# Kernel tuning notes

Hardware: AMD Instinct MI355X
Metric: run time of the kernel (lower is better)

Reference implementation:

```python
import jax, jax.numpy as jnp
import numpy as np

NEG_SLOPE = 0.2
NUM_GRAPHS = 64


def _gatv2_layer(x, src, dst, Wl, bl, Wr, br, att, bias, n_nodes, heads, ch):
    # lin_l (source) and lin_r (target) transforms -> [N, H, C]
    xs = (x @ Wl + bl).reshape(n_nodes, heads, ch)
    xd = (x @ Wr + br).reshape(n_nodes, heads, ch)
    s = xs[src]                                   # [E, H, C] gathered source feats
    e = jax.nn.leaky_relu(s + xd[dst], NEG_SLOPE)  # GATv2: leaky_relu BEFORE att dot
    score = jnp.einsum('ehc,hc->eh', e, att)       # [E, H]
    # segment softmax over edges sharing the same target node
    smax = jax.ops.segment_max(score, dst, num_segments=n_nodes)
    ex = jnp.exp(score - smax[dst])
    denom = jax.ops.segment_sum(ex, dst, num_segments=n_nodes)
    alpha = ex / denom[dst]                        # [E, H]
    out = jax.ops.segment_sum(alpha[:, :, None] * s, dst, num_segments=n_nodes)
    return out.reshape(n_nodes, heads * ch) + bias


def setup_inputs() -> dict:
    key = jax.random.key(0)
    ks = jax.random.split(key, 20)
    N, E, F = 50000, 800000, 128
    H, C = 4, 64
    G = NUM_GRAPHS
    sc = 0.05
    inp = {
        'x': jax.random.normal(ks[0], (N, F), jnp.float32),
        'edge_index': jax.random.randint(ks[1], (2, E), 0, N, jnp.int64 if jax.config.read('jax_enable_x64') else jnp.int32).astype(jnp.int32),
        'batch': jnp.sort(jax.random.randint(ks[2], (N,), 0, G)).astype(jnp.int32),
        'W_l1': jax.random.normal(ks[3], (F, H * C)) * sc,
        'b_l1': jax.random.normal(ks[4], (H * C,)) * sc,
        'W_r1': jax.random.normal(ks[5], (F, H * C)) * sc,
        'b_r1': jax.random.normal(ks[6], (H * C,)) * sc,
        'att1': jax.random.normal(ks[7], (H, C)) * sc,
        'bias1': jax.random.normal(ks[8], (H * C,)) * sc,
        'W_l2': jax.random.normal(ks[9], (H * C, C)) * sc,
        'b_l2': jax.random.normal(ks[10], (C,)) * sc,
        'W_r2': jax.random.normal(ks[11], (H * C, C)) * sc,
        'b_r2': jax.random.normal(ks[12], (C,)) * sc,
        'att2': jax.random.normal(ks[13], (1, C)) * sc,
        'bias2': jax.random.normal(ks[14], (C,)) * sc,
        'W_lin': jax.random.normal(ks[15], (C, 1)) * sc,
        'b_lin': jax.random.normal(ks[16], (1,)) * sc,
    }
    return inp


def reference(x, edge_index, batch, W_l1, b_l1, W_r1, b_r1, att1, bias1,
              W_l2, b_l2, W_r2, b_r2, att2, bias2, W_lin, b_lin):
    N = x.shape[0]
    # PyG GATv2Conv adds self-loops by default
    loops = jnp.arange(N, dtype=edge_index.dtype)
    src = jnp.concatenate([edge_index[0], loops])
    dst = jnp.concatenate([edge_index[1], loops])

    h = _gatv2_layer(x, src, dst, W_l1, b_l1, W_r1, b_r1, att1, bias1, N, 4, 64)
    h = jax.nn.relu(h)  # dropout=identity (eval), norm=Identity
    h = _gatv2_layer(h, src, dst, W_l2, b_l2, W_r2, b_r2, att2, bias2, N, 1, 64)

    # global mean pool over graphs
    sums = jax.ops.segment_sum(h, batch, num_segments=NUM_GRAPHS)
    counts = jax.ops.segment_sum(jnp.ones((N,), h.dtype), batch, num_segments=NUM_GRAPHS)
    pooled = sums / jnp.maximum(counts, 1.0)[:, None]  # [G, 64]
    return pooled @ W_lin + b_lin                      # [G, 1]
```

## Files before the change

kernel.cpp:

```cpp
#include <hip/hip_runtime.h>
#include <hip/hip_bf16.h>
#include <math.h>

typedef __attribute__((ext_vector_type(8))) short short8;
typedef __attribute__((ext_vector_type(4))) float floatx4;

__device__ __forceinline__ float bf2f(unsigned short u) {
  union { unsigned int i; float f; } v; v.i = ((unsigned int)u) << 16; return v.f;
}
__device__ __forceinline__ unsigned short f2bf(float f) {
  union { float f; unsigned int u; } v; v.f = f;
  unsigned int r = (v.u + 0x7fffu + ((v.u >> 16) & 1u)) >> 16;
  return (unsigned short)r;
}
__device__ __forceinline__ int imin(int a, int b) { return a < b ? a : b; }
__device__ __forceinline__ int iclamp(int v, int lo, int hi) {
  return v < lo ? lo : (v > hi ? hi : v);
}
__device__ __forceinline__ float uasf(unsigned int u) {
  union { unsigned int i; float f; } v; v.i = u; return v.f;
}
__device__ __forceinline__ float sum16(float x) {
  union { float f; int i; } a, t;
  a.f = x;
  t.i = __builtin_amdgcn_update_dpp(0, a.i, 0x121, 0xF, 0xF, true); a.f += t.f;
  t.i = __builtin_amdgcn_update_dpp(0, a.i, 0x122, 0xF, 0xF, true); a.f += t.f;
  t.i = __builtin_amdgcn_update_dpp(0, a.i, 0x124, 0xF, 0xF, true); a.f += t.f;
  t.i = __builtin_amdgcn_update_dpp(0, a.i, 0x128, 0xF, 0xF, true); a.f += t.f;
  return a.f;
}

__global__ void k_sentinel(float* out, float val) {
  if (threadIdx.x < 64) out[threadIdx.x] = val;
}

struct CvtSegs {
  const void* src[10];
  unsigned short* dst[10];
  int len[10];
};

__global__ void k_prep(const void* __restrict__ x, unsigned short* __restrict__ x_c,
                       int n8, CvtSegs segs,
                       const void* __restrict__ s0, const void* __restrict__ s1,
                       const void* __restrict__ s2, const void* __restrict__ s3,
                       unsigned short* __restrict__ d0, unsigned short* __restrict__ d1,
                       unsigned short* __restrict__ d2, unsigned short* __restrict__ d3,
                       const int* __restrict__ edst, int* deg, int E, int N,
                       int* dflag, int* colx, int ET, int nCvt8, int nTransB) {
  __shared__ int csh;
  if (threadIdx.x == 0) csh = 0;
  __syncthreads();
  {
    unsigned short u = ((const unsigned short*)x)[threadIdx.x];
    int e = (u >> 7) & 0xFF;
    atomicAdd(&csh, (u == 0) || (e >= 100 && e <= 145));
  }
  __syncthreads();
  int isf = (csh < 240);

  int b = blockIdx.x;
  if (b < nCvt8) {
    if (!isf) return;
    int i = b * 256 + threadIdx.x;
    if (i >= n8) return;
    const float* s = (const float*)x + (size_t)i * 8;
    ushort4 a, c;
    a.x = f2bf(s[0]); a.y = f2bf(s[1]); a.z = f2bf(s[2]); a.w = f2bf(s[3]);
    c.x = f2bf(s[4]); c.y = f2bf(s[5]); c.z = f2bf(s[6]); c.w = f2bf(s[7]);
    ((ushort4*)x_c)[i * 2] = a;
    ((ushort4*)x_c)[i * 2 + 1] = c;
    return;
  }
  b -= nCvt8;
  if (b < 10) {
    if (b == 0) {
      if (threadIdx.x == 0) dflag[0] = isf;
      if (threadIdx.x >= 240) colx[ET + (threadIdx.x - 240)] = 0;
    }
    int i = threadIdx.x;
    if (i < segs.len[b])
      segs.dst[b][i] = isf ? f2bf(((const float*)segs.src[b])[i])
                           : ((const unsigned short*)segs.src[b])[i];
    return;
  }
  b -= 10;
  if (b < nTransB) {
    int idx = b * 256 + threadIdx.x;
    const void* src; unsigned short* dst; int R, C, loc;
    if (idx < 32768)      { src = s0; dst = d0; R = 128; C = 256; loc = idx; }
    else if (idx < 65536) { src = s1; dst = d1; R = 128; C = 256; loc = idx - 32768; }
    else if (idx < 81920) { src = s2; dst = d2; R = 256; C = 64;  loc = idx - 65536; }
    else                  { src = s3; dst = d3; R = 256; C = 64;  loc = idx - 81920; }
    unsigned short u = isf ? f2bf(((const float*)src)[loc])
                           : ((const unsigned short*)src)[loc];
    int r = loc / C, cc = loc - r * C;
    dst[cc * R + r] = u;
    return;
  }
  b -= nTransB;
  int base = b * 1024 + threadIdx.x;
#pragma unroll
  for (int k = 0; k < 4; ++k) {
    int e = base + k * 256;
    if (e < E) atomicAdd(&deg[iclamp(edst[e], 0, N - 1)], 1);
  }
}

__global__ __launch_bounds__(1024) void k_scan1(const int* __restrict__ deg, int* bsum, int N) {
  __shared__ int sm[1024];
  int tid = threadIdx.x;
  int i = blockIdx.x * 1024 + tid;
  sm[tid] = (i < N) ? deg[i] + 1 : 0;
  __syncthreads();
  for (int off = 512; off > 0; off >>= 1) {
    if (tid < off) sm[tid] += sm[tid + off];
    __syncthreads();
  }
  if (tid == 0) bsum[blockIdx.x] = sm[0];
}

__global__ __launch_bounds__(1024) void k_scan3(const int* __restrict__ deg,
                                                const int* __restrict__ bsum,
                                                int* rowptr, int* cursor, int N) {
  __shared__ int sm[1024];
  __shared__ int boff;
  int tid = threadIdx.x;
  if (tid == 0) {
    int r = 0;
    for (int b = 0; b < blockIdx.x; ++b) r += bsum[b];
    boff = r;
  }
  int i = blockIdx.x * 1024 + tid;
  int v = (i < N) ? deg[i] + 1 : 0;
  sm[tid] = v;
  __syncthreads();
  for (int off = 1; off < 1024; off <<= 1) {
    int t = (tid >= off) ? sm[tid - off] : 0;
    __syncthreads();
    sm[tid] += t;
    __syncthreads();
  }
  if (i < N) {
    int ex = sm[tid] - v + boff;
    rowptr[i] = ex;
    cursor[i] = ex;
    if (i == N - 1) rowptr[N] = ex + v;
  }
}

template <int K, int CT, int RT>
__device__ __forceinline__ void gemm2r_body(
    int bx, int by, int tid,
    const unsigned short* __restrict__ A,
    const unsigned short* __restrict__ BTl, const unsigned short* __restrict__ BTr,
    const unsigned short* __restrict__ bl, const unsigned short* __restrict__ br,
    unsigned short* __restrict__ outl, unsigned short* __restrict__ outr,
    int Nrows, int M) {
  constexpr int KI = K / 32;
  int lane = tid & 63;
  int wave = tid >> 6;
  int r = lane & 15, q = lane >> 4;
  int col0 = by * (4 * CT * 16) + wave * (CT * 16);
  int row0 = bx * (16 * RT);
  short8 Bl[KI][CT], Br[KI][CT];
#pragma unroll
  for (int t = 0; t < CT; ++t) {
    const unsigned short* bpl = BTl + (size_t)(col0 + t * 16 + r) * K + q * 8;
    const unsigned short* bpr = BTr + (size_t)(col0 + t * 16 + r) * K + q * 8;
#pragma unroll
    for (int k = 0; k < KI; ++k) {
      Bl[k][t] = *reinterpret_cast<const short8*>(bpl + k * 32);
      Br[k][t] = *reinterpret_cast<const short8*>(bpr + k * 32);
    }
  }
  float bvl[CT], bvr[CT];
#pragma unroll
  for (int t = 0; t < CT; ++t) {
    bvl[t] = bf2f(bl[col0 + t * 16 + r]);
    bvr[t] = bf2f(br[col0 + t * 16 + r]);
  }
  short8 a[KI], an[KI];
  {
    int ar0 = imin(row0 + r, Nrows - 1);
    const unsigned short* Ap = A + (size_t)ar0 * K + q * 8;
#pragma unroll
    for (int k = 0; k < KI; ++k) a[k] = *reinterpret_cast<const short8*>(Ap + k * 32);
  }
  for (int rt = 0; rt < RT; ++rt) {
    if (rt + 1 < RT) {
      int arn = imin(row0 + (rt + 1) * 16 + r, Nrows - 1);
      const unsigned short* Apn = A + (size_t)arn * K + q * 8;
#pragma unroll
      for (int k = 0; k < KI; ++k) an[k] = *reinterpret_cast<const short8*>(Apn + k * 32);
    }
    floatx4 accl[CT], accr[CT];
#pragma unroll
    for (int t = 0; t < CT; ++t) {
      accl[t] = (floatx4){0.f, 0.f, 0.f, 0.f};
      accr[t] = (floatx4){0.f, 0.f, 0.f, 0.f};
    }
#pragma unroll
    for (int k = 0; k < KI; ++k) {
#pragma unroll
      for (int t = 0; t < CT; ++t) {
        accl[t] = __builtin_amdgcn_mfma_f32_16x16x32_bf16(a[k], Bl[k][t], accl[t], 0, 0, 0);
        accr[t] = __builtin_amdgcn_mfma_f32_16x16x32_bf16(a[k], Br[k][t], accr[t], 0, 0, 0);
      }
    }
#pragma unroll
    for (int t = 0; t < CT; ++t) {
      int col = col0 + t * 16 + r;
#pragma unroll
      for (int rr = 0; rr < 4; ++rr) {
        int row = row0 + rt * 16 + q * 4 + rr;
        if (row < Nrows) {
          outl[(size_t)row * M + col] = f2bf(accl[t][rr] + bvl[t]);
          outr[(size_t)row * M + col] = f2bf(accr[t][rr] + bvr[t]);
        }
      }
    }
#pragma unroll
    for (int k = 0; k < KI; ++k) a[k] = an[k];
  }
}

__global__ __launch_bounds__(256) void k_phase1(
    const unsigned short* __restrict__ A0, const unsigned short* __restrict__ A1,
    const int* __restrict__ dflag,
    const unsigned short* __restrict__ BTl, const unsigned short* __restrict__ BTr,
    const unsigned short* __restrict__ bl, const unsigned short* __restrict__ br,
    unsigned short* __restrict__ outl, unsigned short* __restrict__ outr,
    int Nrows, int M, int nG, int nS,
    const int* __restrict__ esrc, const int* __restrict__ edst,
    const int* __restrict__ rowptr, int* cursor, int* colx, int E, int N) {
  int b = blockIdx.x;
  int m2 = 2 * imin(nG, nS);
  bool isG;
  int idx;
  if (b < m2) { isG = (b & 1) == 0; idx = b >> 1; }
  else        { isG = nG > nS;      idx = imin(nG, nS) + (b - m2); }
  if (isG) {
    const unsigned short* A = dflag[0] ? A1 : A0;
    gemm2r_body<128, 2, 8>(idx >> 1, idx & 1, threadIdx.x, A, BTl, BTr, bl, br,
                           outl, outr, Nrows, M);
    return;
  }
  int ET = E + N;
  int base = idx * 1024 + threadIdx.x;
#pragma unroll
  for (int k = 0; k < 4; ++k) {
    int e = base + k * 256;
    if (e < ET) {
      if (e < E) {
        int s = iclamp(esrc[e], 0, N - 1), d = iclamp(edst[e], 0, N - 1);
        int pos = atomicAdd(&cursor[d], 1);
        colx[iclamp(pos, 0, ET - 1)] = s;
      } else {
        int i = e - E;
        colx[rowptr[i + 1] - 1] = i;
      }
    }
  }
}

__global__ __launch_bounds__(256) void k_gemm2r_l2(
    const unsigned short* __restrict__ A,
    const unsigned short* __restrict__ BTl, const unsigned short* __restrict__ BTr,
    const unsigned short* __restrict__ bl, const unsigned short* __restrict__ br,
    unsigned short* __restrict__ outl, unsigned short* __restrict__ outr,
    int Nrows, int M) {
  gemm2r_body<256, 1, 4>(blockIdx.x, 0, threadIdx.x, A, BTl, BTr, bl, br,
                         outl, outr, Nrows, M);
}

#define UNPACK2(u, v0, v1, v2, v3)          \
  v0 = uasf(u.x << 16); v1 = uasf(u.x & 0xffff0000u); \
  v2 = uasf(u.y << 16); v3 = uasf(u.y & 0xffff0000u);

#define SCORE(q0, q1, q2, q3, p)                             \
  p = q0 * 0.6f;                                             \
  p = fmaf(q1, 0.6f, p); p = fmaf(q2, 0.6f, p); p = fmaf(q3, 0.6f, p); \
  p = fmaf(c0, fabsf(q0), p); p = fmaf(c1, fabsf(q1), p);    \
  p = fmaf(c2, fabsf(q2), p); p = fmaf(c3, fabsf(q3), p);

__global__ __launch_bounds__(256) void k_agg_h4(
    const int* __restrict__ rowptr, const int* __restrict__ colx,
    const unsigned short* __restrict__ xs, const unsigned short* __restrict__ xd,
    const unsigned short* __restrict__ att, const unsigned short* __restrict__ bias,
    unsigned short* __restrict__ hout, int N) {
  int lane = threadIdx.x & 63;
  int dst = (blockIdx.x * 256 + threadIdx.x) >> 6;
  if (dst >= N) return;
  int off = lane << 2;
  unsigned int off2 = (unsigned int)off * 2;
  const char* xsb = (const char*)xs;
  ushort4 au = *reinterpret_cast<const ushort4*>(att + off);
  ushort4 du = *reinterpret_cast<const ushort4*>(xd + (size_t)dst * 256 + off);
  float a0 = bf2f(au.x), a1 = bf2f(au.y), a2 = bf2f(au.z), a3 = bf2f(au.w);
  float d0 = bf2f(du.x), d1 = bf2f(du.y), d2 = bf2f(du.z), d3 = bf2f(du.w);
  float ad0 = a0 * d0, ad1 = a1 * d1, ad2 = a2 * d2, ad3 = a3 * d3;
  float c0 = copysignf(0.4f, a0), c1 = copysignf(0.4f, a1);
  float c2 = copysignf(0.4f, a2), c3 = copysignf(0.4f, a3);
  float l = 0.f, o0 = 0.f, o1 = 0.f, o2 = 0.f, o3 = 0.f;
  int beg = __builtin_amdgcn_readfirstlane(rowptr[dst]);
  int end = __builtin_amdgcn_readfirstlane(rowptr[dst + 1]);
  int p0 = colx[beg], p1 = colx[beg + 1], p2 = colx[beg + 2], p3 = colx[beg + 3];
  uint2 ua = *(const uint2*)(xsb + (((unsigned)p0 << 9) + off2));
  uint2 ub = *(const uint2*)(xsb + (((unsigned)p1 << 9) + off2));
  uint2 uc = *(const uint2*)(xsb + (((unsigned)p2 << 9) + off2));
  uint2 ud = *(const uint2*)(xsb + (((unsigned)p3 << 9) + off2));
  int q0 = 0, q1 = 0, q2 = 0, q3 = 0;
  if (beg + 4 < end) {
    q0 = colx[beg + 4]; q1 = colx[beg + 5]; q2 = colx[beg + 6]; q3 = colx[beg + 7];
  }
  for (int e = beg; e < end; e += 4) {
    uint2 na = ua, nb = ub, nc = uc, nd = ud;
    if (e + 4 < end) {
      na = *(const uint2*)(xsb + (((unsigned)q0 << 9) + off2));
      nb = *(const uint2*)(xsb + (((unsigned)q1 << 9) + off2));
      nc = *(const uint2*)(xsb + (((unsigned)q2 << 9) + off2));
      nd = *(const uint2*)(xsb + (((unsigned)q3 << 9) + off2));
    }
    if (e + 8 < end) {
      q0 = colx[e + 8]; q1 = colx[e + 9]; q2 = colx[e + 10]; q3 = colx[e + 11];
    }
    float va0, va1, va2, va3, vb0, vb1, vb2, vb3;
    float vc0, vc1, vc2, vc3, vd0, vd1, vd2, vd3;
    UNPACK2(ua, va0, va1, va2, va3)
    UNPACK2(ub, vb0, vb1, vb2, vb3)
    UNPACK2(uc, vc0, vc1, vc2, vc3)
    UNPACK2(ud, vd0, vd1, vd2, vd3)
    float qa0 = fmaf(a0, va0, ad0), qa1 = fmaf(a1, va1, ad1);
    float qa2 = fmaf(a2, va2, ad2), qa3 = fmaf(a3, va3, ad3);
    float qb0 = fmaf(a0, vb0, ad0), qb1 = fmaf(a1, vb1, ad1);
    float qb2 = fmaf(a2, vb2, ad2), qb3 = fmaf(a3, vb3, ad3);
    float qc0 = fmaf(a0, vc0, ad0), qc1 = fmaf(a1, vc1, ad1);
    float qc2 = fmaf(a2, vc2, ad2), qc3 = fmaf(a3, vc3, ad3);
    float qd0 = fmaf(a0, vd0, ad0), qd1 = fmaf(a1, vd1, ad1);
    float qd2 = fmaf(a2, vd2, ad2), qd3 = fmaf(a3, vd3, ad3);
    float pa, pb, pc, pd;
    SCORE(qa0, qa1, qa2, qa3, pa)
    SCORE(qb0, qb1, qb2, qb3, pb)
    SCORE(qc0, qc1, qc2, qc3, pc)
    SCORE(qd0, qd1, qd2, qd3, pd)
    pa = sum16(pa); pb = sum16(pb); pc = sum16(pc); pd = sum16(pd);
    pa = fminf(pa, 60.f);
    pb = (e + 1 < end) ? fminf(pb, 60.f) : -INFINITY;
    pc = (e + 2 < end) ? fminf(pc, 60.f) : -INFINITY;
    pd = (e + 3 < end) ? fminf(pd, 60.f) : -INFINITY;
    float wa = __expf(pa), wb = __expf(pb), wc = __expf(pc), wd = __expf(pd);
    l += (wa + wb) + (wc + wd);
    o0 = fmaf(wa, va0, o0); o0 = fmaf(wb, vb0, o0);
    o0 = fmaf(wc, vc0, o0); o0 = fmaf(wd, vd0, o0);
    o1 = fmaf(wa, va1, o1); o1 = fmaf(wb, vb1, o1);
    o1 = fmaf(wc, vc1, o1); o1 = fmaf(wd, vd1, o1);
    o2 = fmaf(wa, va2, o2); o2 = fmaf(wb, vb2, o2);
    o2 = fmaf(wc, vc2, o2); o2 = fmaf(wd, vd2, o2);
    o3 = fmaf(wa, va3, o3); o3 = fmaf(wb, vb3, o3);
    o3 = fmaf(wc, vc3, o3); o3 = fmaf(wd, vd3, o3);
    ua = na; ub = nb; uc = nc; ud = nd;
  }
  float rl = 1.0f / l;
  ushort4 bu = *reinterpret_cast<const ushort4*>(bias + off);
  ushort4 res;
  res.x = f2bf(fmaxf(fmaf(o0, rl, bf2f(bu.x)), 0.f));
  res.y = f2bf(fmaxf(fmaf(o1, rl, bf2f(bu.y)), 0.f));
  res.z = f2bf(fmaxf(fmaf(o2, rl, bf2f(bu.z)), 0.f));
  res.w = f2bf(fmaxf(fmaf(o3, rl, bf2f(bu.w)), 0.f));
  *reinterpret_cast<ushort4*>(hout + (size_t)dst * 256 + off) = res;
}

__global__ __launch_bounds__(256) void k_agg_h1(
    const int* __restrict__ rowptr, const int* __restrict__ colx,
    const unsigned short* __restrict__ xs, const unsigned short* __restrict__ xd,
    const unsigned short* __restrict__ att, const unsigned short* __restrict__ bias,
    float* __restrict__ hout, int N) {
  int lane = threadIdx.x & 63;
  int wid = (blockIdx.x * 256 + threadIdx.x) >> 6;
  int g = lane >> 4, sl = lane & 15;
  int dst = wid * 4 + g;
  bool valid = dst < N;
  int dsafe = valid ? dst : 0;
  int cb = sl << 2;
  unsigned int cb2 = (unsigned int)cb * 2;
  const char* xsb = (const char*)xs;
  ushort4 au = *reinterpret_cast<const ushort4*>(att + cb);
  ushort4 du = *reinterpret_cast<const ushort4*>(xd + (size_t)dsafe * 64 + cb);
  float a0 = bf2f(au.x), a1 = bf2f(au.y), a2 = bf2f(au.z), a3 = bf2f(au.w);
  float d0 = bf2f(du.x), d1 = bf2f(du.y), d2 = bf2f(du.z), d3 = bf2f(du.w);
  float ad0 = a0 * d0, ad1 = a1 * d1, ad2 = a2 * d2, ad3 = a3 * d3;
  float c0 = copysignf(0.4f, a0), c1 = copysignf(0.4f, a1);
  float c2 = copysignf(0.4f, a2), c3 = copysignf(0.4f, a3);
  float l = 0.f, o0 = 0.f, o1 = 0.f, o2 = 0.f, o3 = 0.f;
  int beg = valid ? rowptr[dst] : 0;
  int end = valid ? rowptr[dst + 1] : 0;
  if (end > beg) {
    int p0 = colx[beg], p1 = colx[beg + 1], p2 = colx[beg + 2], p3 = colx[beg + 3];
    uint2 ua = *(const uint2*)(xsb + (((unsigned)p0 << 7) + cb2));
    uint2 ub = *(const uint2*)(xsb + (((unsigned)p1 << 7) + cb2));
    uint2 uc = *(const uint2*)(xsb + (((unsigned)p2 << 7) + cb2));
    uint2 ud = *(const uint2*)(xsb + (((unsigned)p3 << 7) + cb2));
    int q0 = 0, q1 = 0, q2 = 0, q3 = 0;
    if (beg + 4 < end) {
      q0 = colx[beg + 4]; q1 = colx[beg + 5]; q2 = colx[beg + 6]; q3 = colx[beg + 7];
    }
    for (int e = beg; e < end; e += 4) {
      uint2 na = ua, nb = ub, nc = uc, nd = ud;
      if (e + 4 < end) {
        na = *(const uint2*)(xsb + (((unsigned)q0 << 7) + cb2));
        nb = *(const uint2*)(xsb + (((unsigned)q1 << 7) + cb2));
        nc = *(const uint2*)(xsb + (((unsigned)q2 << 7) + cb2));
        nd = *(const uint2*)(xsb + (((unsigned)q3 << 7) + cb2));
      }
      if (e + 8 < end) {
        q0 = colx[e + 8]; q1 = colx[e + 9]; q2 = colx[e + 10]; q3 = colx[e + 11];
      }
      float va0, va1, va2, va3, vb0, vb1, vb2, vb3;
      float vc0, vc1, vc2, vc3, vd0, vd1, vd2, vd3;
      UNPACK2(ua, va0, va1, va2, va3)
      UNPACK2(ub, vb0, vb1, vb2, vb3)
      UNPACK2(uc, vc0, vc1, vc2, vc3)
      UNPACK2(ud, vd0, vd1, vd2, vd3)
      float qa0 = fmaf(a0, va0, ad0), qa1 = fmaf(a1, va1, ad1);
      float qa2 = fmaf(a2, va2, ad2), qa3 = fmaf(a3, va3, ad3);
      float qb0 = fmaf(a0, vb0, ad0), qb1 = fmaf(a1, vb1, ad1);
      float qb2 = fmaf(a2, vb2, ad2), qb3 = fmaf(a3, vb3, ad3);
      float qc0 = fmaf(a0, vc0, ad0), qc1 = fmaf(a1, vc1, ad1);
      float qc2 = fmaf(a2, vc2, ad2), qc3 = fmaf(a3, vc3, ad3);
      float qd0 = fmaf(a0, vd0, ad0), qd1 = fmaf(a1, vd1, ad1);
      float qd2 = fmaf(a2, vd2, ad2), qd3 = fmaf(a3, vd3, ad3);
      float pa, pb, pc, pd;
      SCORE(qa0, qa1, qa2, qa3, pa)
      SCORE(qb0, qb1, qb2, qb3, pb)
      SCORE(qc0, qc1, qc2, qc3, pc)
      SCORE(qd0, qd1, qd2, qd3, pd)
      pa = sum16(pa); pb = sum16(pb); pc = sum16(pc); pd = sum16(pd);
      pa = fminf(pa, 60.f);
      pb = (e + 1 < end) ? fminf(pb, 60.f) : -INFINITY;
      pc = (e + 2 < end) ? fminf(pc, 60.f) : -INFINITY;
      pd = (e + 3 < end) ? fminf(pd, 60.f) : -INFINITY;
      float wa = __expf(pa), wb = __expf(pb), wc = __expf(pc), wd = __expf(pd);
      l += (wa + wb) + (wc + wd);
      o0 = fmaf(wa, va0, o0); o0 = fmaf(wb, vb0, o0);
      o0 = fmaf(wc, vc0, o0); o0 = fmaf(wd, vd0, o0);
      o1 = fmaf(wa, va1, o1); o1 = fmaf(wb, vb1, o1);
      o1 = fmaf(wc, vc1, o1); o1 = fmaf(wd, vd1, o1);
      o2 = fmaf(wa, va2, o2); o2 = fmaf(wb, vb2, o2);
      o2 = fmaf(wc, vc2, o2); o2 = fmaf(wd, vd2, o2);
      o3 = fmaf(wa, va3, o3); o3 = fmaf(wb, vb3, o3);
      o3 = fmaf(wc, vc3, o3); o3 = fmaf(wd, vd3, o3);
      ua = na; ub = nb; uc = nc; ud = nd;
    }
  }
  if (valid) {
    float rl = 1.0f / l;
    ushort4 bu = *reinterpret_cast<const ushort4*>(bias + cb);
    floatx4 res;
    res[0] = fmaf(o0, rl, bf2f(bu.x));
    res[1] = fmaf(o1, rl, bf2f(bu.y));
    res[2] = fmaf(o2, rl, bf2f(bu.z));
    res[3] = fmaf(o3, rl, bf2f(bu.w));
    *reinterpret_cast<floatx4*>(hout + (size_t)dst * 64 + cb) = res;
  }
}

__global__ __launch_bounds__(256) void k_pool(const float* __restrict__ h2,
                                              const int* __restrict__ batch,
                                              float* pool, int* cnt, int N) {
  int lane = threadIdx.x & 63;
  int wid = (blockIdx.x * 256 + threadIdx.x) >> 6;
  int n0 = wid * 32;
  if (n0 >= N) return;
  int nend = imin(n0 + 32, N);
  float acc = 0.f;
  int c = 0;
  int gcur = iclamp(batch[n0], 0, 63);
  for (int n = n0; n < nend; ++n) {
    int gg = iclamp(batch[n], 0, 63);
    if (gg != gcur) {
      atomicAdd(&pool[gcur * 64 + lane], acc);
      if (lane == 0) atomicAdd(&cnt[gcur], c);
      acc = 0.f; c = 0; gcur = gg;
    }
    acc += h2[(size_t)n * 64 + lane];
    c++;
  }
  atomicAdd(&pool[gcur * 64 + lane], acc);
  if (lane == 0) atomicAdd(&cnt[gcur], c);
}

__global__ void k_final(const float* __restrict__ pool, const int* __restrict__ cnt,
                        const unsigned short* __restrict__ Wlinc,
                        const unsigned short* __restrict__ blinc,
                        float* __restrict__ out) {
  int g = threadIdx.x;
  if (g >= 64) return;
  float inv = 1.f / fmaxf((float)cnt[g], 1.f);
  float s = 0.f;
  for (int c = 0; c < 64; ++c) s += pool[g * 64 + c] * bf2f(Wlinc[c]);
  out[g] = fmaf(s, inv, bf2f(blinc[0]));
}

extern "C" void kernel_launch(void* const* d_in, const int* in_sizes, int n_in,
                              void* d_out, int out_size, void* d_ws, size_t ws_size,
                              hipStream_t stream) {
  const void* x     = d_in[0];
  const int*  ei    = (const int*)d_in[1];
  const int*  batch = (const int*)d_in[2];
  const void* Wl1 = d_in[3];  const void* bl1 = d_in[4];
  const void* Wr1 = d_in[5];  const void* br1 = d_in[6];
  const void* att1 = d_in[7]; const void* bias1 = d_in[8];
  const void* Wl2 = d_in[9];  const void* bl2 = d_in[10];
  const void* Wr2 = d_in[11]; const void* br2 = d_in[12];
  const void* att2 = d_in[13]; const void* bias2 = d_in[14];
  const void* Wlin = d_in[15]; const void* blin = d_in[16];
  float* out = (float*)d_out;

  const int F = 128, HC = 256, C2 = 64;
  int N = in_sizes[0] / F;
  int E = in_sizes[1] / 2;
  int ET = E + N;
  const int* esrc = ei;
  const int* edst = ei + E;

  char* w = (char*)d_ws;
  auto alloc = [&](size_t bytes) {
    char* p = w;
    w += (bytes + 255) & ~(size_t)255;
    return p;
  };
  int* dflag  = (int*)alloc(4);
  int* rowptr = (int*)alloc((size_t)(N + 1) * 4);
  int* cursor = (int*)alloc((size_t)N * 4);
  int* bsum   = (int*)alloc(1024 * 4);
  int* colx   = (int*)alloc((size_t)(ET + 16) * 4);
  unsigned short* smallc = (unsigned short*)alloc(4096);
  unsigned short* Wl1T = (unsigned short*)alloc((size_t)F * HC * 2);
  unsigned short* Wr1T = (unsigned short*)alloc((size_t)F * HC * 2);
  unsigned short* Wl2T = (unsigned short*)alloc((size_t)HC * C2 * 2);
  unsigned short* Wr2T = (unsigned short*)alloc((size_t)HC * C2 * 2);
  int* deg    = (int*)alloc((size_t)N * 4);
  float* pool = (float*)alloc(64 * 64 * 4);
  int* cnt    = (int*)alloc(64 * 4);
  unsigned short* xs1  = (unsigned short*)alloc((size_t)N * HC * 2);
  unsigned short* xd1  = (unsigned short*)alloc((size_t)N * HC * 2);
  unsigned short* h1   = (unsigned short*)alloc((size_t)N * HC * 2);
  size_t required = (size_t)(w - (char*)d_ws);
  size_t zlen = (size_t)((char*)cnt + 256 - (char*)deg);

  unsigned short* x_c = h1;
  unsigned short* xs2 = xs1;
  unsigned short* xd2 = xs1 + (size_t)N * C2;
  float*          h2  = (float*)xd1;

  unsigned short* bl1c   = smallc + 0;
  unsigned short* br1c   = smallc + 256;
  unsigned short* att1c  = smallc + 512;
  unsigned short* bias1c = smallc + 768;
  unsigned short* bl2c   = smallc + 1024;
  unsigned short* br2c   = smallc + 1088;
  unsigned short* att2c  = smallc + 1152;
  unsigned short* bias2c = smallc + 1216;
  unsigned short* Wlinc  = smallc + 1280;
  unsigned short* blinc  = smallc + 1344;

  if (ws_size < required) {
    k_sentinel<<<1, 64, 0, stream>>>(out, 1000.f + (float)(ws_size >> 20));
    return;
  }

  hipMemsetAsync(deg, 0, zlen, stream);

  CvtSegs segs;
  const void* ssrc[10] = {bl1, br1, att1, bias1, bl2, br2, att2, bias2, Wlin, blin};
  unsigned short* sdst[10] = {bl1c, br1c, att1c, bias1c, bl2c, br2c, att2c, bias2c, Wlinc, blinc};
  int slen[10] = {256, 256, 256, 256, 64, 64, 64, 64, 64, 1};
  for (int i = 0; i < 10; ++i) { segs.src[i] = ssrc[i]; segs.dst[i] = sdst[i]; segs.len[i] = slen[i]; }
  int n8 = N * F / 8;
  int nCvt8 = (n8 + 255) / 256;
  int nTransB = (2 * F * HC + 2 * HC * C2 + 255) / 256;
  int nHist = (E + 1023) / 1024;
  k_prep<<<nCvt8 + 10 + nTransB + nHist, 256, 0, stream>>>(
      x, x_c, n8, segs, Wl1, Wr1, Wl2, Wr2, Wl1T, Wr1T, Wl2T, Wr2T,
      edst, deg, E, N, dflag, colx, ET, nCvt8, nTransB);

  int nb = (N + 1023) / 1024;
  k_scan1<<<nb, 1024, 0, stream>>>(deg, bsum, N);
  k_scan3<<<nb, 1024, 0, stream>>>(deg, bsum, rowptr, cursor, N);

  int nG = ((N + 127) / 128) * 2;
  int nS = (ET + 1023) / 1024;
  k_phase1<<<nG + nS, 256, 0, stream>>>(
      (const unsigned short*)x, x_c, dflag, Wl1T, Wr1T, bl1c, br1c, xs1, xd1,
      N, HC, nG, nS, esrc, edst, rowptr, cursor, colx, E, N);

  k_agg_h4<<<(N + 3) / 4, 256, 0, stream>>>(rowptr, colx, xs1, xd1, att1c, bias1c, h1, N);

  k_gemm2r_l2<<<(N + 63) / 64, 256, 0, stream>>>(h1, Wl2T, Wr2T, bl2c, br2c, xs2, xd2, N, C2);
  k_agg_h1<<<(N + 15) / 16, 256, 0, stream>>>(rowptr, colx, xs2, xd2, att2c, bias2c, h2, N);

  int pw = (N + 31) / 32;
  k_pool<<<(pw + 3) / 4, 256, 0, stream>>>(h2, batch, pool, cnt, N);
  k_final<<<1, 64, 0, stream>>>(pool, cnt, Wlinc, blinc, out);
}
```

Measured before the change: 328.9 us.

## Pad CSR rows to multiples of four and vectorize aggregation index loads

Each CSR row is now padded to a multiple of four entries, with the padding filled with node 0. This lets the aggregation kernels load neighbor indices as aligned int4 vectors and run a branch-free loop of 8 edges per step. The attention vector is pre-scaled by log2(e) (folded into float copies) so scores feed the hardware exp2 directly, and the leaky-relu constants are rescaled to match. Launch bounds now request more waves per SIMD. The cost is extra gather traffic for padded entries, which are masked to zero weight, plus a padding-fill loop in the CSR build.

```diff
diff --git a/kernel.cpp b/kernel.cpp
--- a/kernel.cpp
+++ b/kernel.cpp
@@ -4,6 +4,11 @@
 
 typedef __attribute__((ext_vector_type(8))) short short8;
 typedef __attribute__((ext_vector_type(4))) float floatx4;
+typedef __attribute__((ext_vector_type(4))) int intx4;
+
+#define ATT_SCALE 0.865617024533378f
+#define C_ABS 0.6666666666667f
+#define PCLAMP 86.5f
 
 __device__ __forceinline__ float bf2f(unsigned short u) {
   union { unsigned int i; float f; } v; v.i = ((unsigned int)u) << 16; return v.f;
@@ -19,6 +24,13 @@
 }
 __device__ __forceinline__ float uasf(unsigned int u) {
   union { unsigned int i; float f; } v; v.i = u; return v.f;
+}
+__device__ __forceinline__ float exp2fast(float x) {
+#if __has_builtin(__builtin_amdgcn_exp2f)
+  return __builtin_amdgcn_exp2f(x);
+#else
+  return exp2f(x);
+#endif
 }
 __device__ __forceinline__ float sum16(float x) {
   union { float f; int i; } a, t;
@@ -47,7 +59,8 @@
                        unsigned short* __restrict__ d0, unsigned short* __restrict__ d1,
                        unsigned short* __restrict__ d2, unsigned short* __restrict__ d3,
                        const int* __restrict__ edst, int* deg, int E, int N,
-                       int* dflag, int* colx, int ET, int nCvt8, int nTransB) {
+                       int* dflag, float* __restrict__ att1s, float* __restrict__ att2s,
+                       int nCvt8, int nTransB) {
   __shared__ int csh;
   if (threadIdx.x == 0) csh = 0;
   __syncthreads();
@@ -74,14 +87,15 @@
   }
   b -= nCvt8;
   if (b < 10) {
-    if (b == 0) {
-      if (threadIdx.x == 0) dflag[0] = isf;
-      if (threadIdx.x >= 240) colx[ET + (threadIdx.x - 240)] = 0;
-    }
+    if (b == 0 && threadIdx.x == 0) dflag[0] = isf;
     int i = threadIdx.x;
-    if (i < segs.len[b])
-      segs.dst[b][i] = isf ? f2bf(((const float*)segs.src[b])[i])
-                           : ((const unsigned short*)segs.src[b])[i];
+    if (i < segs.len[b]) {
+      float v = isf ? ((const float*)segs.src[b])[i]
+                    : bf2f(((const unsigned short*)segs.src[b])[i]);
+      segs.dst[b][i] = f2bf(v);
+      if (b == 2) att1s[i] = v * ATT_SCALE;
+      if (b == 6) att2s[i] = v * ATT_SCALE;
+    }
     return;
   }
   b -= 10;
@@ -111,7 +125,7 @@
   __shared__ int sm[1024];
   int tid = threadIdx.x;
   int i = blockIdx.x * 1024 + tid;
-  sm[tid] = (i < N) ? deg[i] + 1 : 0;
+  sm[tid] = (i < N) ? ((deg[i] + 4) & ~3) : 0;
   __syncthreads();
   for (int off = 512; off > 0; off >>= 1) {
     if (tid < off) sm[tid] += sm[tid + off];
@@ -132,7 +146,7 @@
     boff = r;
   }
   int i = blockIdx.x * 1024 + tid;
-  int v = (i < N) ? deg[i] + 1 : 0;
+  int v = (i < N) ? ((deg[i] + 4) & ~3) : 0;
   sm[tid] = v;
   __syncthreads();
   for (int off = 1; off < 1024; off <<= 1) {
@@ -233,7 +247,8 @@
     unsigned short* __restrict__ outl, unsigned short* __restrict__ outr,
     int Nrows, int M, int nG, int nS,
     const int* __restrict__ esrc, const int* __restrict__ edst,
-    const int* __restrict__ rowptr, int* cursor, int* colx, int E, int N) {
+    const int* __restrict__ rowptr, const int* __restrict__ deg,
+    int* cursor, int* colx, int E, int N) {
   int b = blockIdx.x;
   int m2 = 2 * imin(nG, nS);
   bool isG;
@@ -247,6 +262,7 @@
     return;
   }
   int ET = E + N;
+  int ETcap = E + 4 * N;
   int base = idx * 1024 + threadIdx.x;
 #pragma unroll
   for (int k = 0; k < 4; ++k) {
@@ -255,10 +271,17 @@
       if (e < E) {
         int s = iclamp(esrc[e], 0, N - 1), d = iclamp(edst[e], 0, N - 1);
         int pos = atomicAdd(&cursor[d], 1);
-        colx[iclamp(pos, 0, ET - 1)] = s;
+        colx[iclamp(pos, 0, ETcap - 1)] = s;
       } else {
         int i = e - E;
-        colx[rowptr[i + 1] - 1] = i;
+        int bg = rowptr[i];
+        int en = bg + deg[i];
+        colx[en] = i;
+        int cap = rowptr[i + 1];
+        for (int j = en + 1; j < cap; ++j) colx[j] = 0;
+        if (i == N - 1) {
+          for (int j = cap; j < cap + 16; ++j) colx[j] = 0;
+        }
       }
     }
   }
@@ -278,16 +301,59 @@
   v0 = uasf(u.x << 16); v1 = uasf(u.x & 0xffff0000u); \
   v2 = uasf(u.y << 16); v3 = uasf(u.y & 0xffff0000u);
 
-#define SCORE(q0, q1, q2, q3, p)                             \
-  p = q0 * 0.6f;                                             \
-  p = fmaf(q1, 0.6f, p); p = fmaf(q2, 0.6f, p); p = fmaf(q3, 0.6f, p); \
-  p = fmaf(c0, fabsf(q0), p); p = fmaf(c1, fabsf(q1), p);    \
-  p = fmaf(c2, fabsf(q2), p); p = fmaf(c3, fabsf(q3), p);
-
-__global__ __launch_bounds__(256) void k_agg_h4(
-    const int* __restrict__ rowptr, const int* __restrict__ colx,
+#define AGG4(U0, U1, U2, U3, E0, F0)                                         \
+  {                                                                          \
+    float va0, va1, va2, va3, vb0, vb1, vb2, vb3;                            \
+    float vc0, vc1, vc2, vc3, vd0, vd1, vd2, vd3;                            \
+    UNPACK2(U0, va0, va1, va2, va3)                                          \
+    UNPACK2(U1, vb0, vb1, vb2, vb3)                                          \
+    UNPACK2(U2, vc0, vc1, vc2, vc3)                                          \
+    UNPACK2(U3, vd0, vd1, vd2, vd3)                                          \
+    float qa0 = fmaf(a0, va0, ad0), qa1 = fmaf(a1, va1, ad1);                \
+    float qa2 = fmaf(a2, va2, ad2), qa3 = fmaf(a3, va3, ad3);                \
+    float qb0 = fmaf(a0, vb0, ad0), qb1 = fmaf(a1, vb1, ad1);                \
+    float qb2 = fmaf(a2, vb2, ad2), qb3 = fmaf(a3, vb3, ad3);                \
+    float qc0 = fmaf(a0, vc0, ad0), qc1 = fmaf(a1, vc1, ad1);                \
+    float qc2 = fmaf(a2, vc2, ad2), qc3 = fmaf(a3, vc3, ad3);                \
+    float qd0 = fmaf(a0, vd0, ad0), qd1 = fmaf(a1, vd1, ad1);                \
+    float qd2 = fmaf(a2, vd2, ad2), qd3 = fmaf(a3, vd3, ad3);                \
+    float pa = (qa0 + qa1) + (qa2 + qa3);                                    \
+    float pb = (qb0 + qb1) + (qb2 + qb3);                                    \
+    float pc = (qc0 + qc1) + (qc2 + qc3);                                    \
+    float pd = (qd0 + qd1) + (qd2 + qd3);                                    \
+    pa = fmaf(c0, fabsf(qa0), pa); pa = fmaf(c1, fabsf(qa1), pa);            \
+    pa = fmaf(c2, fabsf(qa2), pa); pa = fmaf(c3, fabsf(qa3), pa);            \
+    pb = fmaf(c0, fabsf(qb0), pb); pb = fmaf(c1, fabsf(qb1), pb);            \
+    pb = fmaf(c2, fabsf(qb2), pb); pb = fmaf(c3, fabsf(qb3), pb);            \
+    pc = fmaf(c0, fabsf(qc0), pc); pc = fmaf(c1, fabsf(qc1), pc);            \
+    pc = fmaf(c2, fabsf(qc2), pc); pc = fmaf(c3, fabsf(qc3), pc);            \
+    pd = fmaf(c0, fabsf(qd0), pd); pd = fmaf(c1, fabsf(qd1), pd);            \
+    pd = fmaf(c2, fabsf(qd2), pd); pd = fmaf(c3, fabsf(qd3), pd);            \
+    pa = sum16(pa); pb = sum16(pb); pc = sum16(pc); pd = sum16(pd);          \
+    float l0 = (F0) ? PCLAMP : (((E0) < end) ? PCLAMP : -INFINITY);          \
+    float l1 = ((E0) + 1 < end) ? PCLAMP : -INFINITY;                        \
+    float l2 = ((E0) + 2 < end) ? PCLAMP : -INFINITY;                        \
+    float l3 = ((E0) + 3 < end) ? PCLAMP : -INFINITY;                        \
+    pa = fminf(pa, l0); pb = fminf(pb, l1);                                  \
+    pc = fminf(pc, l2); pd = fminf(pd, l3);                                  \
+    float wa = exp2fast(pa), wb = exp2fast(pb);                              \
+    float wc = exp2fast(pc), wd = exp2fast(pd);                              \
+    l += (wa + wb) + (wc + wd);                                              \
+    o0 = fmaf(wa, va0, o0); o0 = fmaf(wb, vb0, o0);                          \
+    o0 = fmaf(wc, vc0, o0); o0 = fmaf(wd, vd0, o0);                          \
+    o1 = fmaf(wa, va1, o1); o1 = fmaf(wb, vb1, o1);                          \
+    o1 = fmaf(wc, vc1, o1); o1 = fmaf(wd, vd1, o1);                          \
+    o2 = fmaf(wa, va2, o2); o2 = fmaf(wb, vb2, o2);                          \
+    o2 = fmaf(wc, vc2, o2); o2 = fmaf(wd, vd2, o2);                          \
+    o3 = fmaf(wa, va3, o3); o3 = fmaf(wb, vb3, o3);                          \
+    o3 = fmaf(wc, vc3, o3); o3 = fmaf(wd, vd3, o3);                          \
+  }
+
+__global__ __launch_bounds__(256, 6) void k_agg_h4(
+    const int* __restrict__ rowptr, const int* __restrict__ deg,
+    const int* __restrict__ colx,
     const unsigned short* __restrict__ xs, const unsigned short* __restrict__ xd,
-    const unsigned short* __restrict__ att, const unsigned short* __restrict__ bias,
+    const float* __restrict__ atts, const unsigned short* __restrict__ bias,
     unsigned short* __restrict__ hout, int N) {
   int lane = threadIdx.x & 63;
   int dst = (blockIdx.x * 256 + threadIdx.x) >> 6;
@@ -295,72 +361,31 @@
   int off = lane << 2;
   unsigned int off2 = (unsigned int)off * 2;
   const char* xsb = (const char*)xs;
-  ushort4 au = *reinterpret_cast<const ushort4*>(att + off);
+  floatx4 av = *reinterpret_cast<const floatx4*>(atts + off);
   ushort4 du = *reinterpret_cast<const ushort4*>(xd + (size_t)dst * 256 + off);
-  float a0 = bf2f(au.x), a1 = bf2f(au.y), a2 = bf2f(au.z), a3 = bf2f(au.w);
+  float a0 = av[0], a1 = av[1], a2 = av[2], a3 = av[3];
   float d0 = bf2f(du.x), d1 = bf2f(du.y), d2 = bf2f(du.z), d3 = bf2f(du.w);
   float ad0 = a0 * d0, ad1 = a1 * d1, ad2 = a2 * d2, ad3 = a3 * d3;
-  float c0 = copysignf(0.4f, a0), c1 = copysignf(0.4f, a1);
-  float c2 = copysignf(0.4f, a2), c3 = copysignf(0.4f, a3);
+  float c0 = copysignf(C_ABS, a0), c1 = copysignf(C_ABS, a1);
+  float c2 = copysignf(C_ABS, a2), c3 = copysignf(C_ABS, a3);
   float l = 0.f, o0 = 0.f, o1 = 0.f, o2 = 0.f, o3 = 0.f;
   int beg = __builtin_amdgcn_readfirstlane(rowptr[dst]);
-  int end = __builtin_amdgcn_readfirstlane(rowptr[dst + 1]);
-  int p0 = colx[beg], p1 = colx[beg + 1], p2 = colx[beg + 2], p3 = colx[beg + 3];
-  uint2 ua = *(const uint2*)(xsb + (((unsigned)p0 << 9) + off2));
-  uint2 ub = *(const uint2*)(xsb + (((unsigned)p1 << 9) + off2));
-  uint2 uc = *(const uint2*)(xsb + (((unsigned)p2 << 9) + off2));
-  uint2 ud = *(const uint2*)(xsb + (((unsigned)p3 << 9) + off2));
-  int q0 = 0, q1 = 0, q2 = 0, q3 = 0;
-  if (beg + 4 < end) {
-    q0 = colx[beg + 4]; q1 = colx[beg + 5]; q2 = colx[beg + 6]; q3 = colx[beg + 7];
-  }
-  for (int e = beg; e < end; e += 4) {
-    uint2 na = ua, nb = ub, nc = uc, nd = ud;
-    if (e + 4 < end) {
-      na = *(const uint2*)(xsb + (((unsigned)q0 << 9) + off2));
-      nb = *(const uint2*)(xsb + (((unsigned)q1 << 9) + off2));
-      nc = *(const uint2*)(xsb + (((unsigned)q2 << 9) + off2));
-      nd = *(const uint2*)(xsb + (((unsigned)q3 << 9) + off2));
-    }
-    if (e + 8 < end) {
-      q0 = colx[e + 8]; q1 = colx[e + 9]; q2 = colx[e + 10]; q3 = colx[e + 11];
-    }
-    float va0, va1, va2, va3, vb0, vb1, vb2, vb3;
-    float vc0, vc1, vc2, vc3, vd0, vd1, vd2, vd3;
-    UNPACK2(ua, va0, va1, va2, va3)
-    UNPACK2(ub, vb0, vb1, vb2, vb3)
-    UNPACK2(uc, vc0, vc1, vc2, vc3)
-    UNPACK2(ud, vd0, vd1, vd2, vd3)
-    float qa0 = fmaf(a0, va0, ad0), qa1 = fmaf(a1, va1, ad1);
-    float qa2 = fmaf(a2, va2, ad2), qa3 = fmaf(a3, va3, ad3);
-    float qb0 = fmaf(a0, vb0, ad0), qb1 = fmaf(a1, vb1, ad1);
-    float qb2 = fmaf(a2, vb2, ad2), qb3 = fmaf(a3, vb3, ad3);
-    float qc0 = fmaf(a0, vc0, ad0), qc1 = fmaf(a1, vc1, ad1);
-    float qc2 = fmaf(a2, vc2, ad2), qc3 = fmaf(a3, vc3, ad3);
-    float qd0 = fmaf(a0, vd0, ad0), qd1 = fmaf(a1, vd1, ad1);
-    float qd2 = fmaf(a2, vd2, ad2), qd3 = fmaf(a3, vd3, ad3);
-    float pa, pb, pc, pd;
-    SCORE(qa0, qa1, qa2, qa3, pa)
-    SCORE(qb0, qb1, qb2, qb3, pb)
-    SCORE(qc0, qc1, qc2, qc3, pc)
-    SCORE(qd0, qd1, qd2, qd3, pd)
-    pa = sum16(pa); pb = sum16(pb); pc = sum16(pc); pd = sum16(pd);
-    pa = fminf(pa, 60.f);
-    pb = (e + 1 < end) ? fminf(pb, 60.f) : -INFINITY;
-    pc = (e + 2 < end) ? fminf(pc, 60.f) : -INFINITY;
-    pd = (e + 3 < end) ? fminf(pd, 60.f) : -INFINITY;
-    float wa = __expf(pa), wb = __expf(pb), wc = __expf(pc), wd = __expf(pd);
-    l += (wa + wb) + (wc + wd);
-    o0 = fmaf(wa, va0, o0); o0 = fmaf(wb, vb0, o0);
-    o0 = fmaf(wc, vc0, o0); o0 = fmaf(wd, vd0, o0);
-    o1 = fmaf(wa, va1, o1); o1 = fmaf(wb, vb1, o1);
-    o1 = fmaf(wc, vc1, o1); o1 = fmaf(wd, vd1, o1);
-    o2 = fmaf(wa, va2, o2); o2 = fmaf(wb, vb2, o2);
-    o2 = fmaf(wc, vc2, o2); o2 = fmaf(wd, vd2, o2);
-    o3 = fmaf(wa, va3, o3); o3 = fmaf(wb, vb3, o3);
-    o3 = fmaf(wc, vc3, o3); o3 = fmaf(wd, vd3, o3);
-    ua = na; ub = nb; uc = nc; ud = nd;
-  }
+  int cnt = __builtin_amdgcn_readfirstlane(deg[dst]) + 1;
+  int end = beg + cnt;
+#define GATH(p) (*(const uint2*)(xsb + (((unsigned)(p) << 9) + off2)))
+  intx4 pA = *(const intx4*)(colx + beg);
+  intx4 pB = *(const intx4*)(colx + beg + 4);
+  uint2 ua = GATH(pA.x), ub = GATH(pA.y), uc = GATH(pA.z), ud = GATH(pA.w);
+  uint2 ue = GATH(pB.x), uf = GATH(pB.y), ug = GATH(pB.z), uh = GATH(pB.w);
+  for (int e = beg; e < end; e += 8) {
+    intx4 pC = *(const intx4*)(colx + e + 8);
+    intx4 pD = *(const intx4*)(colx + e + 12);
+    AGG4(ua, ub, uc, ud, e, 1)
+    ua = GATH(pC.x); ub = GATH(pC.y); uc = GATH(pC.z); ud = GATH(pC.w);
+    AGG4(ue, uf, ug, uh, e + 4, 0)
+    ue = GATH(pD.x); uf = GATH(pD.y); ug = GATH(pD.z); uh = GATH(pD.w);
+  }
+#undef GATH
   float rl = 1.0f / l;
   ushort4 bu = *reinterpret_cast<const ushort4*>(bias + off);
   ushort4 res;
@@ -371,10 +396,11 @@
   *reinterpret_cast<ushort4*>(hout + (size_t)dst * 256 + off) = res;
 }
 
-__global__ __launch_bounds__(256) void k_agg_h1(
-    const int* __restrict__ rowptr, const int* __restrict__ colx,
+__global__ __launch_bounds__(256, 6) void k_agg_h1(
+    const int* __restrict__ rowptr, const int* __restrict__ deg,
+    const int* __restrict__ colx,
     const unsigned short* __restrict__ xs, const unsigned short* __restrict__ xd,
-    const unsigned short* __restrict__ att, const unsigned short* __restrict__ bias,
+    const float* __restrict__ atts, const unsigned short* __restrict__ bias,
     float* __restrict__ hout, int N) {
   int lane = threadIdx.x & 63;
   int wid = (blockIdx.x * 256 + threadIdx.x) >> 6;
@@ -385,74 +411,30 @@
   int cb = sl << 2;
   unsigned int cb2 = (unsigned int)cb * 2;
   const char* xsb = (const char*)xs;
-  ushort4 au = *reinterpret_cast<const ushort4*>(att + cb);
+  floatx4 av = *reinterpret_cast<const floatx4*>(atts + cb);
   ushort4 du = *reinterpret_cast<const ushort4*>(xd + (size_t)dsafe * 64 + cb);
-  float a0 = bf2f(au.x), a1 = bf2f(au.y), a2 = bf2f(au.z), a3 = bf2f(au.w);
+  float a0 = av[0], a1 = av[1], a2 = av[2], a3 = av[3];
   float d0 = bf2f(du.x), d1 = bf2f(du.y), d2 = bf2f(du.z), d3 = bf2f(du.w);
   float ad0 = a0 * d0, ad1 = a1 * d1, ad2 = a2 * d2, ad3 = a3 * d3;
-  float c0 = copysignf(0.4f, a0), c1 = copysignf(0.4f, a1);
-  float c2 = copysignf(0.4f, a2), c3 = copysignf(0.4f, a3);
+  float c0 = copysignf(C_ABS, a0), c1 = copysignf(C_ABS, a1);
+  float c2 = copysignf(C_ABS, a2), c3 = copysignf(C_ABS, a3);
   float l = 0.f, o0 = 0.f, o1 = 0.f, o2 = 0.f, o3 = 0.f;
   int beg = valid ? rowptr[dst] : 0;
-  int end = valid ? rowptr[dst + 1] : 0;
-  if (end > beg) {
-    int p0 = colx[beg], p1 = colx[beg + 1], p2 = colx[beg + 2], p3 = colx[beg + 3];
-    uint2 ua = *(const uint2*)(xsb + (((unsigned)p0 << 7) + cb2));
-    uint2 ub = *(const uint2*)(xsb + (((unsigned)p1 << 7) + cb2));
-    uint2 uc = *(const uint2*)(xsb + (((unsigned)p2 << 7) + cb2));
-    uint2 ud = *(const uint2*)(xsb + (((unsigned)p3 << 7) + cb2));
-    int q0 = 0, q1 = 0, q2 = 0, q3 = 0;
-    if (beg + 4 < end) {
-      q0 = colx[beg + 4]; q1 = colx[beg + 5]; q2 = colx[beg + 6]; q3 = colx[beg + 7];
-    }
-    for (int e = beg; e < end; e += 4) {
-      uint2 na = ua, nb = ub, nc = uc, nd = ud;
-      if (e + 4 < end) {
-        na = *(const uint2*)(xsb + (((unsigned)q0 << 7) + cb2));
-        nb = *(const uint2*)(xsb + (((unsigned)q1 << 7) + cb2));
-        nc = *(const uint2*)(xsb + (((unsigned)q2 << 7) + cb2));
-        nd = *(const uint2*)(xsb + (((unsigned)q3 << 7) + cb2));
-      }
-      if (e + 8 < end) {
-        q0 = colx[e + 8]; q1 = colx[e + 9]; q2 = colx[e + 10]; q3 = colx[e + 11];
-      }
-      float va0, va1, va2, va3, vb0, vb1, vb2, vb3;
-      float vc0, vc1, vc2, vc3, vd0, vd1, vd2, vd3;
-      UNPACK2(ua, va0, va1, va2, va3)
-      UNPACK2(ub, vb0, vb1, vb2, vb3)
-      UNPACK2(uc, vc0, vc1, vc2, vc3)
-      UNPACK2(ud, vd0, vd1, vd2, vd3)
-      float qa0 = fmaf(a0, va0, ad0), qa1 = fmaf(a1, va1, ad1);
-      float qa2 = fmaf(a2, va2, ad2), qa3 = fmaf(a3, va3, ad3);
-      float qb0 = fmaf(a0, vb0, ad0), qb1 = fmaf(a1, vb1, ad1);
-      float qb2 = fmaf(a2, vb2, ad2), qb3 = fmaf(a3, vb3, ad3);
-      float qc0 = fmaf(a0, vc0, ad0), qc1 = fmaf(a1, vc1, ad1);
-      float qc2 = fmaf(a2, vc2, ad2), qc3 = fmaf(a3, vc3, ad3);
-      float qd0 = fmaf(a0, vd0, ad0), qd1 = fmaf(a1, vd1, ad1);
-      float qd2 = fmaf(a2, vd2, ad2), qd3 = fmaf(a3, vd3, ad3);
-      float pa, pb, pc, pd;
-      SCORE(qa0, qa1, qa2, qa3, pa)
-      SCORE(qb0, qb1, qb2, qb3, pb)
-      SCORE(qc0, qc1, qc2, qc3, pc)
-      SCORE(qd0, qd1, qd2, qd3, pd)
-      pa = sum16(pa); pb = sum16(pb); pc = sum16(pc); pd = sum16(pd);
-      pa = fminf(pa, 60.f);
-      pb = (e + 1 < end) ? fminf(pb, 60.f) : -INFINITY;
-      pc = (e + 2 < end) ? fminf(pc, 60.f) : -INFINITY;
-      pd = (e + 3 < end) ? fminf(pd, 60.f) : -INFINITY;
-      float wa = __expf(pa), wb = __expf(pb), wc = __expf(pc), wd = __expf(pd);
-      l += (wa + wb) + (wc + wd);
-      o0 = fmaf(wa, va0, o0); o0 = fmaf(wb, vb0, o0);
-      o0 = fmaf(wc, vc0, o0); o0 = fmaf(wd, vd0, o0);
-      o1 = fmaf(wa, va1, o1); o1 = fmaf(wb, vb1, o1);
-      o1 = fmaf(wc, vc1, o1); o1 = fmaf(wd, vd1, o1);
-      o2 = fmaf(wa, va2, o2); o2 = fmaf(wb, vb2, o2);
-      o2 = fmaf(wc, vc2, o2); o2 = fmaf(wd, vd2, o2);
-      o3 = fmaf(wa, va3, o3); o3 = fmaf(wb, vb3, o3);
-      o3 = fmaf(wc, vc3, o3); o3 = fmaf(wd, vd3, o3);
-      ua = na; ub = nb; uc = nc; ud = nd;
-    }
-  }
+  int end = beg + (valid ? deg[dst] + 1 : 0);
+#define GATH(p) (*(const uint2*)(xsb + (((unsigned)(p) << 7) + cb2)))
+  intx4 pA = *(const intx4*)(colx + beg);
+  intx4 pB = *(const intx4*)(colx + beg + 4);
+  uint2 ua = GATH(pA.x), ub = GATH(pA.y), uc = GATH(pA.z), ud = GATH(pA.w);
+  uint2 ue = GATH(pB.x), uf = GATH(pB.y), ug = GATH(pB.z), uh = GATH(pB.w);
+  for (int e = beg; e < end; e += 8) {
+    intx4 pC = *(const intx4*)(colx + e + 8);
+    intx4 pD = *(const intx4*)(colx + e + 12);
+    AGG4(ua, ub, uc, ud, e, 1)
+    ua = GATH(pC.x); ub = GATH(pC.y); uc = GATH(pC.z); ud = GATH(pC.w);
+    AGG4(ue, uf, ug, uh, e + 4, 0)
+    ue = GATH(pD.x); uf = GATH(pD.y); ug = GATH(pD.z); uh = GATH(pD.w);
+  }
+#undef GATH
   if (valid) {
     float rl = 1.0f / l;
     ushort4 bu = *reinterpret_cast<const ushort4*>(bias + cb);
@@ -534,8 +516,10 @@
   int* rowptr = (int*)alloc((size_t)(N + 1) * 4);
   int* cursor = (int*)alloc((size_t)N * 4);
   int* bsum   = (int*)alloc(1024 * 4);
-  int* colx   = (int*)alloc((size_t)(ET + 16) * 4);
+  int* colx   = (int*)alloc((size_t)(E + 4 * N + 16) * 4);
   unsigned short* smallc = (unsigned short*)alloc(4096);
+  float* att1s = (float*)alloc(256 * 4);
+  float* att2s = (float*)alloc(64 * 4);
   unsigned short* Wl1T = (unsigned short*)alloc((size_t)F * HC * 2);
   unsigned short* Wr1T = (unsigned short*)alloc((size_t)F * HC * 2);
   unsigned short* Wl2T = (unsigned short*)alloc((size_t)HC * C2 * 2);
@@ -583,7 +567,7 @@
   int nHist = (E + 1023) / 1024;
   k_prep<<<nCvt8 + 10 + nTransB + nHist, 256, 0, stream>>>(
       x, x_c, n8, segs, Wl1, Wr1, Wl2, Wr2, Wl1T, Wr1T, Wl2T, Wr2T,
-      edst, deg, E, N, dflag, colx, ET, nCvt8, nTransB);
+      edst, deg, E, N, dflag, att1s, att2s, nCvt8, nTransB);
 
   int nb = (N + 1023) / 1024;
   k_scan1<<<nb, 1024, 0, stream>>>(deg, bsum, N);
@@ -593,12 +577,12 @@
   int nS = (ET + 1023) / 1024;
   k_phase1<<<nG + nS, 256, 0, stream>>>(
       (const unsigned short*)x, x_c, dflag, Wl1T, Wr1T, bl1c, br1c, xs1, xd1,
-      N, HC, nG, nS, esrc, edst, rowptr, cursor, colx, E, N);
-
-  k_agg_h4<<<(N + 3) / 4, 256, 0, stream>>>(rowptr, colx, xs1, xd1, att1c, bias1c, h1, N);
+      N, HC, nG, nS, esrc, edst, rowptr, deg, cursor, colx, E, N);
+
+  k_agg_h4<<<(N + 3) / 4, 256, 0, stream>>>(rowptr, deg, colx, xs1, xd1, att1s, bias1c, h1, N);
 
   k_gemm2r_l2<<<(N + 63) / 64, 256, 0, stream>>>(h1, Wl2T, Wr2T, bl2c, br2c, xs2, xd2, N, C2);
-  k_agg_h1<<<(N + 15) / 16, 256, 0, stream>>>(rowptr, colx, xs2, xd2, att2c, bias2c, h2, N);
+  k_agg_h1<<<(N + 15) / 16, 256, 0, stream>>>(rowptr, deg, colx, xs2, xd2, att2s, bias2c, h2, N);
 
   int pw = (N + 31) / 32;
   k_pool<<<(pw + 3) / 4, 256, 0, stream>>>(h2, batch, pool, cnt, N);
```

New measurement: 333.6 us. About the same (+1.4%).
